# Performance work log

Measured on AMD Instinct MI355X. Metric: run time of the kernel, lower is better.

The kernel has to match this reference:

```python
import jax, jax.numpy as jnp
import numpy as np
from jax import lax

B, C, HW = 256, 3, 128
OC, K = 16, 3
NH, FANIN, NO = 256, 512, 10
F = OC * 63 * 63  # 63504 flattened features after conv(k=3,valid)->pool(2)


def setup_inputs() -> dict:
    key = jax.random.key(0)
    ks = jax.random.split(key, 8)
    inputs = jax.random.normal(ks[0], (B, C, HW, HW), dtype=jnp.float32)
    conv_w = jax.random.normal(ks[1], (OC, C, K, K), dtype=jnp.float32) * 0.1
    conv_b = jax.random.normal(ks[2], (OC,), dtype=jnp.float32) * 0.1
    hidden_idx = jax.random.randint(ks[3], (NH, FANIN), 0, F, dtype=jnp.int64 if jax.config.jax_enable_x64 else jnp.int32)
    hidden_w = jax.random.normal(ks[4], (NH, FANIN), dtype=jnp.float32) * (1.0 / np.sqrt(FANIN))
    hidden_b = jax.random.normal(ks[5], (NH,), dtype=jnp.float32) * 0.1
    out_w = jax.random.normal(ks[6], (NO, NH), dtype=jnp.float32) * (1.0 / np.sqrt(NH))
    out_b = jax.random.normal(ks[7], (NO,), dtype=jnp.float32) * 0.1
    return {"inputs": inputs, "conv_w": conv_w, "conv_b": conv_b,
            "hidden_idx": hidden_idx, "hidden_w": hidden_w, "hidden_b": hidden_b,
            "out_w": out_w, "out_b": out_b}


def reference(inputs, conv_w, conv_b, hidden_idx, hidden_w, hidden_b, out_w, out_b):
    # --- feature extraction: conv(valid) -> relu -> maxpool(2) -> flatten ---
    x = lax.conv_general_dilated(inputs, conv_w, window_strides=(1, 1), padding='VALID',
                                 dimension_numbers=('NCHW', 'OIHW', 'NCHW'))
    x = jax.nn.relu(x + conv_b[None, :, None, None])            # [B, OC, 126, 126]
    x = lax.reduce_window(x, -jnp.inf, lax.max,
                          window_dimensions=(1, 1, 2, 2),
                          window_strides=(1, 1, 2, 2), padding='VALID')  # [B, OC, 63, 63]
    feats = x.reshape(x.shape[0], -1)                           # [B, F] (row-major == torch.flatten)
    # --- NEAT-style classification: per-node gather -> tiny linear -> sigmoid ---
    gathered = feats[:, hidden_idx]                             # [B, NH, FANIN] irregular gather
    hidden = jax.nn.sigmoid(jnp.einsum('bhk,hk->bh', gathered, hidden_w) + hidden_b)  # [B, NH]
    out = jax.nn.sigmoid(hidden @ out_w.T + out_b)              # [B, NO]
    return out
```

## Files before the change

kernel.cpp:

```cpp
#include <hip/hip_runtime.h>
#include <hip/hip_fp16.h>
#include <math.h>

#define BATCH 256
#define CIN 3
#define HW 128
#define OC 16
#define POOLED 63
#define FEAT 63504
#define NH 256
#define FANIN 512
#define NO 10
#define CHW (CIN*HW*HW)

#define PADX 134
#define ROWS 15

typedef _Float16 h4 __attribute__((ext_vector_type(4)));
typedef float    f4 __attribute__((ext_vector_type(4)));

__global__ __launch_bounds__(256) void conv_pool_kernel(const float* __restrict__ inp,
                                                        const float* __restrict__ cw,
                                                        const float* __restrict__ cb,
                                                        __half* __restrict__ featsT) {
    __shared__ _Float16 sB[ROWS * 16 * PADX];
    const int t    = threadIdx.x;
    const int l    = t & 63;
    const int w    = t >> 6;
    const int q    = l >> 4;
    const int bcol = l & 15;

    const int id = blockIdx.x;
    const int u  = id & 7;
    const int v  = id >> 3;
    const int i  = v >> 1;
    const int g  = 2 * u + (v & 1);
    const int y0 = 2 * i;

    {
        unsigned int* z = (unsigned int*)&sB[192 * PADX];
        const int nd = (ROWS * 16 - 192) * PADX / 2;
        for (int zz = t; zz < nd; zz += 256) z[zz] = 0u;
    }

#pragma unroll
    for (int bb = 0; bb < 4; ++bb) {
        const int b_l = w * 4 + bb;
#pragma unroll
        for (int rr = 0; rr < 12; ++rr) {
            const int c  = rr >> 2;
            const int dy = rr & 3;
            const float2 vv = *(const float2*)
                &inp[((size_t)(g * 16 + b_l) * CIN + c) * (HW * HW) + (y0 + dy) * HW + 2 * l];
            *(__half2*)&sB[(size_t)((c * 4 + dy) * 16 + b_l) * PADX + 2 * l] =
                __float22half2_rn(vv);
        }
    }
    __syncthreads();

    h4 aLo, aHi;
    int P[8];
    float bias[4];
#pragma unroll
    for (int m = 0; m < 8; ++m) {
        const int k  = (m < 4) ? (4 * q + m) : (16 + 4 * q + (m - 4));
        const int c  = (k * 57) >> 9;
        const int r2 = k - 9 * c;
        const int ky = (r2 * 11) >> 5;
        const int kx = r2 - 3 * ky;
        P[m] = ((c * 4 + ky) * 16 + bcol) * PADX + kx;
        const float wv = (k < 27) ? cw[bcol * 27 + k] : 0.0f;
        if (m < 4) aLo[m] = (_Float16)wv; else aHi[m - 4] = (_Float16)wv;
    }
#pragma unroll
    for (int r = 0; r < 4; ++r) bias[r] = cb[4 * q + r];

    const int jend = (16 * w + 16 < 63) ? (16 * w + 16) : 63;
    for (int j = 16 * w; j < jend; ++j) {
        f4 d[2][2];
#pragma unroll
        for (int ys = 0; ys < 2; ++ys)
#pragma unroll
            for (int xs = 0; xs < 2; ++xs) {
                const int U = ys * (16 * PADX) + 2 * j + xs;
                h4 bLo, bHi;
#pragma unroll
                for (int jj = 0; jj < 4; ++jj) {
                    bLo[jj] = sB[P[jj]     + U];
                    bHi[jj] = sB[P[4 + jj] + U];
                }
                f4 acc = {0.f, 0.f, 0.f, 0.f};
                acc = __builtin_amdgcn_mfma_f32_16x16x16f16(aLo, bLo, acc, 0, 0, 0);
                acc = __builtin_amdgcn_mfma_f32_16x16x16f16(aHi, bHi, acc, 0, 0, 0);
                d[ys][xs] = acc;
            }
#pragma unroll
        for (int r = 0; r < 4; ++r) {
            const float m0 = fmaxf(d[0][0][r], d[0][1][r]);
            const float m1 = fmaxf(d[1][0][r], d[1][1][r]);
            const float mv = fmaxf(m0, m1);
            const float rv = fmaxf(mv + bias[r], 0.0f);
            const int oc = 4 * q + r;
            featsT[(size_t)(oc * 3969 + i * POOLED + j) * BATCH + g * 16 + bcol] =
                __float2half_rn(rv);
        }
    }
}

__global__ __launch_bounds__(256) void hidden_kernel(const __half* __restrict__ featsT,
                                                     const int* __restrict__ hidx,
                                                     const float* __restrict__ hw,
                                                     float* __restrict__ hiddenP) {
    __shared__ int   sidx[128];
    __shared__ float swt[128];
    __shared__ float red[4][256];
    const int h = blockIdx.x;
    const int q = blockIdx.y;
    const int t = threadIdx.x;
    if (t < 128) {
        sidx[t] = hidx[h * FANIN + q * 128 + t];
        swt[t]  = hw[h * FANIN + q * 128 + t];
    }
    __syncthreads();

    const int lane = t & 63;
    const int w    = t >> 6;
    float a0 = 0.f, a1 = 0.f, a2 = 0.f, a3 = 0.f;
#pragma unroll 16
    for (int kk = 0; kk < 32; ++kk) {
        const int k = w * 32 + kk;
        const __half2* rp =
            reinterpret_cast<const __half2*>(featsT + (size_t)sidx[k] * BATCH) + 2 * lane;
        const __half2 p0 = rp[0];
        const __half2 p1 = rp[1];
        const float2 f0 = __half22float2(p0);
        const float2 f1 = __half22float2(p1);
        const float  wt = swt[k];
        a0 += f0.x * wt; a1 += f0.y * wt; a2 += f1.x * wt; a3 += f1.y * wt;
    }
    red[w][4 * lane + 0] = a0;
    red[w][4 * lane + 1] = a1;
    red[w][4 * lane + 2] = a2;
    red[w][4 * lane + 3] = a3;
    __syncthreads();

    if (t < 256) {
        const float s = red[0][t] + red[1][t] + red[2][t] + red[3][t];
        hiddenP[((size_t)q * NH + h) * BATCH + t] = s;
    }
}

__global__ __launch_bounds__(256) void out_kernel(const float* __restrict__ hiddenP,
                                                  const float* __restrict__ hb,
                                                  const float* __restrict__ ow,
                                                  const float* __restrict__ ob,
                                                  float* __restrict__ out) {
    __shared__ float red[256];
    const int o  = blockIdx.x;
    const int bt = blockIdx.y;
    const int tb = threadIdx.x & 15;
    const int hg = threadIdx.x >> 4;
    const int b  = bt * 16 + tb;
    float acc = 0.f;
#pragma unroll
    for (int k = 0; k < 16; ++k) {
        const int h = hg * 16 + k;
        const float s = hiddenP[(0 * NH + h) * BATCH + b]
                      + hiddenP[(1 * NH + h) * BATCH + b]
                      + hiddenP[(2 * NH + h) * BATCH + b]
                      + hiddenP[(3 * NH + h) * BATCH + b] + hb[h];
        const float hs = 1.0f / (1.0f + __expf(-s));
        acc += hs * ow[o * NH + h];
    }
    red[threadIdx.x] = acc;
    __syncthreads();
    if (hg == 0) {
        float s = 0.f;
#pragma unroll
        for (int gg = 0; gg < 16; ++gg) s += red[gg * 16 + tb];
        out[b * NO + o] = 1.0f / (1.0f + __expf(-(s + ob[o])));
    }
}

extern "C" void kernel_launch(void* const* d_in, const int* in_sizes, int n_in,
                              void* d_out, int out_size, void* d_ws, size_t ws_size,
                              hipStream_t stream) {
    const float* inputs   = (const float*)d_in[0];
    const float* conv_w   = (const float*)d_in[1];
    const float* conv_b   = (const float*)d_in[2];
    const int*   hidden_i = (const int*)d_in[3];
    const float* hidden_w = (const float*)d_in[4];
    const float* hidden_b = (const float*)d_in[5];
    const float* out_w    = (const float*)d_in[6];
    const float* out_b    = (const float*)d_in[7];
    float* out = (float*)d_out;

    char* ws = (char*)d_ws;
    __half* featsT  = (__half*)ws;
    float*  hiddenP = (float*)(ws + (size_t)FEAT * BATCH * 2);

    conv_pool_kernel<<<1008, 256, 0, stream>>>(inputs, conv_w, conv_b, featsT);
    hidden_kernel<<<dim3(NH, 4), 256, 0, stream>>>(featsT, hidden_i, hidden_w, hiddenP);
    out_kernel<<<dim3(NO, 16), 256, 0, stream>>>(hiddenP, hidden_b, out_w, out_b, out);
}
```

Before: 139.0 us.

## Restructure conv MFMA as row-wise Toeplitz and widen hidden gather loads

The conv kernel now splits the 3x3x3 reduction into three row slices, each holding the three kx weights shifted into two Toeplitz-style A fragments, so each MFMA produces two output columns from one contiguous 4-half B vector. This replaces the scattered per-element LDS gathers and lets the 16-row shared buffer drop its zero-padding rows and clearing loop. The hidden kernel loads 16 bytes per lane, with two half-waves each covering a different fanin index, then combines them with a cross-lane shuffle, so fewer and wider global gather loads are issued. MFMA count per pooled output rises from 8 to 12 in exchange for cheaper operand loads.

```diff
diff --git a/kernel.cpp b/kernel.cpp
--- a/kernel.cpp
+++ b/kernel.cpp
@@ -11,12 +11,12 @@
 #define NH 256
 #define FANIN 512
 #define NO 10
-#define CHW (CIN*HW*HW)
 
 #define PADX 134
-#define ROWS 15
+#define ROWS 12
 
 typedef _Float16 h4 __attribute__((ext_vector_type(4)));
+typedef _Float16 h2v __attribute__((ext_vector_type(2)));
 typedef float    f4 __attribute__((ext_vector_type(4)));
 
 __global__ __launch_bounds__(256) void conv_pool_kernel(const float* __restrict__ inp,
@@ -37,12 +37,6 @@
     const int g  = 2 * u + (v & 1);
     const int y0 = 2 * i;
 
-    {
-        unsigned int* z = (unsigned int*)&sB[192 * PADX];
-        const int nd = (ROWS * 16 - 192) * PADX / 2;
-        for (int zz = t; zz < nd; zz += 256) z[zz] = 0u;
-    }
-
 #pragma unroll
     for (int bb = 0; bb < 4; ++bb) {
         const int b_l = w * 4 + bb;
@@ -58,47 +52,51 @@
     }
     __syncthreads();
 
-    h4 aLo, aHi;
-    int P[8];
+    h4  aF[3][2];
+    int bOff[3][2];
     float bias[4];
 #pragma unroll
-    for (int m = 0; m < 8; ++m) {
-        const int k  = (m < 4) ? (4 * q + m) : (16 + 4 * q + (m - 4));
-        const int c  = (k * 57) >> 9;
-        const int r2 = k - 9 * c;
-        const int ky = (r2 * 11) >> 5;
-        const int kx = r2 - 3 * ky;
-        P[m] = ((c * 4 + ky) * 16 + bcol) * PADX + kx;
-        const float wv = (k < 27) ? cw[bcol * 27 + k] : 0.0f;
-        if (m < 4) aLo[m] = (_Float16)wv; else aHi[m - 4] = (_Float16)wv;
+    for (int s = 0; s < 3; ++s) {
+        const int rIdx = s * 4 + q;
+        const int c    = (rIdx * 11) >> 5;
+        const int ky   = rIdx - 3 * c;
+        const bool valid = (c < 3);
+        float wv[3];
+#pragma unroll
+        for (int kx = 0; kx < 3; ++kx)
+            wv[kx] = valid ? cw[(bcol * CIN + c) * 9 + ky * 3 + kx] : 0.0f;
+        aF[s][0][0] = (_Float16)wv[0]; aF[s][0][1] = (_Float16)wv[1];
+        aF[s][0][2] = (_Float16)wv[2]; aF[s][0][3] = (_Float16)0.0f;
+        aF[s][1][0] = (_Float16)0.0f;  aF[s][1][1] = (_Float16)wv[0];
+        aF[s][1][2] = (_Float16)wv[1]; aF[s][1][3] = (_Float16)wv[2];
+#pragma unroll
+        for (int ys = 0; ys < 2; ++ys) {
+            const int row = valid ? (c * 4 + ys + ky) : ys;
+            bOff[s][ys] = (row * 16 + bcol) * PADX;
+        }
     }
 #pragma unroll
     for (int r = 0; r < 4; ++r) bias[r] = cb[4 * q + r];
 
     const int jend = (16 * w + 16 < 63) ? (16 * w + 16) : 63;
     for (int j = 16 * w; j < jend; ++j) {
-        f4 d[2][2];
-#pragma unroll
-        for (int ys = 0; ys < 2; ++ys)
-#pragma unroll
-            for (int xs = 0; xs < 2; ++xs) {
-                const int U = ys * (16 * PADX) + 2 * j + xs;
-                h4 bLo, bHi;
-#pragma unroll
-                for (int jj = 0; jj < 4; ++jj) {
-                    bLo[jj] = sB[P[jj]     + U];
-                    bHi[jj] = sB[P[4 + jj] + U];
-                }
-                f4 acc = {0.f, 0.f, 0.f, 0.f};
-                acc = __builtin_amdgcn_mfma_f32_16x16x16f16(aLo, bLo, acc, 0, 0, 0);
-                acc = __builtin_amdgcn_mfma_f32_16x16x16f16(aHi, bHi, acc, 0, 0, 0);
-                d[ys][xs] = acc;
-            }
+        f4 d00 = {0.f,0.f,0.f,0.f}, d01 = d00, d10 = d00, d11 = d00;
+#pragma unroll
+        for (int s = 0; s < 3; ++s) {
+            const _Float16* p0 = &sB[bOff[s][0] + 2 * j];
+            const _Float16* p1 = &sB[bOff[s][1] + 2 * j];
+            const h2v a0 = *(const h2v*)p0, a1 = *(const h2v*)(p0 + 2);
+            const h2v c0 = *(const h2v*)p1, c1 = *(const h2v*)(p1 + 2);
+            const h4 bF0 = {a0[0], a0[1], a1[0], a1[1]};
+            const h4 bF1 = {c0[0], c0[1], c1[0], c1[1]};
+            d00 = __builtin_amdgcn_mfma_f32_16x16x16f16(aF[s][0], bF0, d00, 0, 0, 0);
+            d01 = __builtin_amdgcn_mfma_f32_16x16x16f16(aF[s][1], bF0, d01, 0, 0, 0);
+            d10 = __builtin_amdgcn_mfma_f32_16x16x16f16(aF[s][0], bF1, d10, 0, 0, 0);
+            d11 = __builtin_amdgcn_mfma_f32_16x16x16f16(aF[s][1], bF1, d11, 0, 0, 0);
+        }
 #pragma unroll
         for (int r = 0; r < 4; ++r) {
-            const float m0 = fmaxf(d[0][0][r], d[0][1][r]);
-            const float m1 = fmaxf(d[1][0][r], d[1][1][r]);
-            const float mv = fmaxf(m0, m1);
+            const float mv = fmaxf(fmaxf(d00[r], d01[r]), fmaxf(d10[r], d11[r]));
             const float rv = fmaxf(mv + bias[r], 0.0f);
             const int oc = 4 * q + r;
             featsT[(size_t)(oc * 3969 + i * POOLED + j) * BATCH + g * 16 + bcol] =
@@ -123,25 +121,30 @@
     }
     __syncthreads();
 
-    const int lane = t & 63;
-    const int w    = t >> 6;
-    float a0 = 0.f, a1 = 0.f, a2 = 0.f, a3 = 0.f;
-#pragma unroll 16
-    for (int kk = 0; kk < 32; ++kk) {
-        const int k = w * 32 + kk;
-        const __half2* rp =
-            reinterpret_cast<const __half2*>(featsT + (size_t)sidx[k] * BATCH) + 2 * lane;
-        const __half2 p0 = rp[0];
-        const __half2 p1 = rp[1];
-        const float2 f0 = __half22float2(p0);
-        const float2 f1 = __half22float2(p1);
-        const float  wt = swt[k];
-        a0 += f0.x * wt; a1 += f0.y * wt; a2 += f1.x * wt; a3 += f1.y * wt;
-    }
-    red[w][4 * lane + 0] = a0;
-    red[w][4 * lane + 1] = a1;
-    red[w][4 * lane + 2] = a2;
-    red[w][4 * lane + 3] = a3;
+    const int l   = t & 63;
+    const int w   = t >> 6;
+    const int hl  = l & 31;
+    const int sel = l >> 5;
+    float acc[8] = {0.f,0.f,0.f,0.f,0.f,0.f,0.f,0.f};
+#pragma unroll
+    for (int m = 0; m < 16; ++m) {
+        const int kloc = w * 32 + 2 * m + sel;
+        const uint4 v = *(const uint4*)(featsT + (size_t)sidx[kloc] * BATCH + 8 * hl);
+        const __half2* hp = reinterpret_cast<const __half2*>(&v);
+        const float wt = swt[kloc];
+#pragma unroll
+        for (int d2 = 0; d2 < 4; ++d2) {
+            const float2 f = __half22float2(hp[d2]);
+            acc[2 * d2 + 0] += f.x * wt;
+            acc[2 * d2 + 1] += f.y * wt;
+        }
+    }
+#pragma unroll
+    for (int e = 0; e < 8; ++e) acc[e] += __shfl_xor(acc[e], 32);
+    if (sel == 0) {
+#pragma unroll
+        for (int e = 0; e < 8; ++e) red[w][8 * hl + e] = acc[e];
+    }
     __syncthreads();
 
     if (t < 256) {
```

Result: faster. 135.0 us (-2.9%).
